# Optimization experiments

Hardware: AMD Instinct MI355X
Metric: run time of the kernel (lower is better)

Reference implementation:

```python
import jax, jax.numpy as jnp
import numpy as np

N_USER = 100000
N_RECIPE = 50000
E = 1000000
H = 128


def setup_inputs() -> dict:
    key = jax.random.key(0)
    ks = jax.random.split(key, 5)
    z_user = jax.random.normal(ks[0], (N_USER, H), dtype=jnp.float32)
    z_recipe = jax.random.normal(ks[1], (N_RECIPE, H), dtype=jnp.float32)
    edge_label_index = jax.random.randint(ks[2], (2, E), 0, N_RECIPE, dtype=jnp.int64)
    W1 = jax.random.normal(ks[3], (2 * H, H), dtype=jnp.float32) * (1.0 / np.sqrt(2 * H))
    b1 = jnp.zeros((H,), dtype=jnp.float32)
    W2 = jax.random.normal(ks[4], (H, 1), dtype=jnp.float32) * (1.0 / np.sqrt(H))
    b2 = jnp.zeros((1,), dtype=jnp.float32)
    return {"z_user": z_user, "z_recipe": z_recipe,
            "edge_label_index": edge_label_index,
            "W1": W1, "b1": b1, "W2": W2, "b2": b2}


def reference(z_user, z_recipe, edge_label_index, W1, b1, W2, b2):
    row, col = edge_label_index[0], edge_label_index[1]
    # gather + concat: [E, 2H]
    z = jnp.concatenate([z_user[row], z_recipe[col]], axis=-1)
    h = jax.nn.relu(z @ W1 + b1)        # [E, H]
    out = h @ W2 + b2                    # [E, 1]
    return out.reshape(-1)
```

## Files before the change

kernel.cpp:

```cpp
#include <hip/hip_runtime.h>
#include <hip/hip_bf16.h>


#define HDIM 128

typedef __attribute__((ext_vector_type(8))) __bf16 bf16x8;
typedef __attribute__((ext_vector_type(16))) float f32x16;

static __device__ __forceinline__ unsigned short bf16_bits(float x) {
  return __builtin_bit_cast(unsigned short, static_cast<__bf16>(x));
}

static __device__ __forceinline__ float bf2f(unsigned short u) {
  return __builtin_bit_cast(float, ((unsigned int)u) << 16);
}

static __device__ __forceinline__ bf16x8 cvt8(float4 a, float4 b) {
  bf16x8 r;
  r[0] = static_cast<__bf16>(a.x);
  r[1] = static_cast<__bf16>(a.y);
  r[2] = static_cast<__bf16>(a.z);
  r[3] = static_cast<__bf16>(a.w);
  r[4] = static_cast<__bf16>(b.x);
  r[5] = static_cast<__bf16>(b.y);
  r[6] = static_cast<__bf16>(b.z);
  r[7] = static_cast<__bf16>(b.w);
  return r;
}

__global__ __launch_bounds__(256) void prep(const float* __restrict__ W1,
                                            unsigned short* __restrict__ W1bf,
                                            const int* __restrict__ eidx, int E,
                                            int* __restrict__ maxarr) {
  const int tid = threadIdx.x;
  const int b = blockIdx.x;
  if (b < 16 && W1bf) {
#pragma unroll
    for (int it = 0; it < 8; ++it) {
      const int idx = (b << 11) + (it << 8) + tid;
      const int k = idx >> 7;
      const int n = idx & 127;
      const int kc = k >> 4;
      const int q = (k >> 3) & 1;
      const int j = k & 7;
      const int nt = n >> 5;
      const int ln = (q << 5) | (n & 31);
      W1bf[((((kc << 2) + nt) << 6) | ln) * 8 + j] = bf16_bits(W1[idx]);
    }
  }
  int local = -1;
  for (int i = b * 256 + tid; i < E; i += 64 * 256)
    local = max(local, eidx[i]);
#pragma unroll
  for (int st = 1; st <= 32; st <<= 1)
    local = max(local, __shfl_xor(local, st));
  __shared__ int wmax[4];
  if ((tid & 63) == 0) wmax[tid >> 6] = local;
  __syncthreads();
  if (tid == 0) {
    int m = max(max(wmax[0], wmax[1]), max(wmax[2], wmax[3]));
    maxarr[b] = m;
  }
}

__global__ __launch_bounds__(256, 4) void proj_nodes(
    const float* __restrict__ zu, int NU, const float* __restrict__ zr, int NR,
    const float* __restrict__ W1, const unsigned short* __restrict__ W1bf,
    const int* __restrict__ maxarr,
    unsigned short* __restrict__ Hu, unsigned short* __restrict__ Hr,
    int ublocks) {
  __shared__ unsigned short Bsw[16384];
  const int tid = threadIdx.x;
  const bool isU = (int)blockIdx.x < ublocks;
  const int kc0 = isU ? 0 : 8;

  if (W1bf) {
    const uint4* s4 = (const uint4*)(W1bf + (kc0 << 11));
    uint4* d4 = (uint4*)Bsw;
#pragma unroll
    for (int i = 0; i < 8; ++i) d4[(i << 8) + tid] = s4[(i << 8) + tid];
  } else {
    const int n = tid & 127;
    const int kh = tid >> 7;
    const int nt = n >> 5;
    const int nl = n & 31;
#pragma unroll 8
    for (int it = 0; it < 64; ++it) {
      const int kl = 2 * it + kh;
      const float w = W1[(kc0 * 16 + kl) * HDIM + n];
      const int kc = kl >> 4;
      const int q = (kl >> 3) & 1;
      const int j = kl & 7;
      const int ln = (q << 5) | nl;
      Bsw[((((kc << 2) + nt) << 6) | ln) * 8 + j] = bf16_bits(w);
    }
  }
  __syncthreads();

  const int lane = tid & 63;
  const int wid = tid >> 6;
  const int m = lane & 31;
  const int half = lane >> 5;
  const int koff = half * 8;

  const int wbase = (isU ? (int)blockIdx.x : (int)blockIdx.x - ublocks) * 4 + wid;
  const int ntiles = isU ? ((NU + 31) >> 5) : ((NR + 31) >> 5);
  const int wstride = (isU ? ublocks : ((int)gridDim.x - ublocks)) * 4;

  int vmax = 0x7fffffff;
  if (isU && maxarr) {
    int v = maxarr[lane];
#pragma unroll
    for (int st = 1; st <= 32; st <<= 1) v = max(v, __shfl_xor(v, st));
    vmax = v;
  }

  const int nmax = isU ? NU : NR;
  const float* zsrc = isU ? zu : zr;
  unsigned short* H = isU ? Hu : Hr;

  for (int t = wbase; t < ntiles; t += wstride) {
    const int base = t << 5;
    if (isU && base > vmax) continue;
    int node = base + m;
    if (node >= nmax) node = nmax - 1;
    const float* src = zsrc + (size_t)node * HDIM + koff;

    f32x16 acc[4];
#pragma unroll
    for (int nt = 0; nt < 4; ++nt) acc[nt] = (f32x16)0.0f;

#pragma unroll
    for (int kcl = 0; kcl < 8; ++kcl) {
      const float4* sa = (const float4*)(src + kcl * 16);
      const bf16x8 a = cvt8(sa[0], sa[1]);
#pragma unroll
      for (int nt = 0; nt < 4; ++nt) {
        const uint4* bp =
            (const uint4*)(Bsw + ((((kcl << 2) + nt) << 6) | lane) * 8);
        const bf16x8 bfr = __builtin_bit_cast(bf16x8, *bp);
        acc[nt] = __builtin_amdgcn_mfma_f32_32x32x16_bf16(a, bfr, acc[nt], 0, 0, 0);
      }
    }

#pragma unroll
    for (int nt = 0; nt < 4; ++nt) {
#pragma unroll
      for (int r = 0; r < 16; ++r) {
        const int row = (r & 3) + ((r >> 2) << 3) + (half << 2);
        const int nrow = base + row;
        if (nrow < nmax)
          H[(size_t)nrow * HDIM + (nt << 5) + m] = bf16_bits(acc[nt][r]);
      }
    }
  }
}

static __device__ __forceinline__ float dot8(uint4 a, uint4 b,
                                             const float* b1c,
                                             const float* w2c) {
  const unsigned short* pa = (const unsigned short*)&a;
  const unsigned short* pb = (const unsigned short*)&b;
  float s = 0.f;
#pragma unroll
  for (int j = 0; j < 8; ++j) {
    const float h = bf2f(pa[j]) + bf2f(pb[j]) + b1c[j];
    s = fmaf(fmaxf(h, 0.f), w2c[j], s);
  }
  return s;
}

__global__ __launch_bounds__(256, 4) void edge_pass(
    const unsigned short* __restrict__ Hu, const unsigned short* __restrict__ Hr,
    const int* __restrict__ eidx, const float* __restrict__ b1,
    const float* __restrict__ W2, const float* __restrict__ b2,
    float* __restrict__ out, int E, int eBeg, int eEnd) {
  const int tid = threadIdx.x;
  const int lane = tid & 63;
  const int c = lane & 15;
  const int g = lane >> 4;
  const int wid = blockIdx.x * 4 + (tid >> 6);
  const int stride = gridDim.x * 4 * 16;

  float b1c[8], w2c[8];
#pragma unroll
  for (int j = 0; j < 8; ++j) {
    b1c[j] = b1[c * 8 + j];
    w2c[j] = W2[c * 8 + j];
  }
  const float b2v = b2[0];
  const int co = c * 8;

  int e = eBeg + wid * 16 + g * 4;
  if (e >= eEnd) return;
  int iu0 = eidx[e],     ir0 = eidx[E + e];
  int iu1 = eidx[e + 1], ir1 = eidx[E + e + 1];
  int iu2 = eidx[e + 2], ir2 = eidx[E + e + 2];
  int iu3 = eidx[e + 3], ir3 = eidx[E + e + 3];

  while (true) {
    const int en = e + stride;
    const bool more = en < eEnd;
    const int ep = more ? en : e;

    const uint4 au0 = *(const uint4*)(Hu + (size_t)iu0 * HDIM + co);
    const uint4 ar0 = *(const uint4*)(Hr + (size_t)ir0 * HDIM + co);
    const uint4 au1 = *(const uint4*)(Hu + (size_t)iu1 * HDIM + co);
    const uint4 ar1 = *(const uint4*)(Hr + (size_t)ir1 * HDIM + co);
    const uint4 au2 = *(const uint4*)(Hu + (size_t)iu2 * HDIM + co);
    const uint4 ar2 = *(const uint4*)(Hr + (size_t)ir2 * HDIM + co);
    const uint4 au3 = *(const uint4*)(Hu + (size_t)iu3 * HDIM + co);
    const uint4 ar3 = *(const uint4*)(Hr + (size_t)ir3 * HDIM + co);

    const int niu0 = eidx[ep],     nir0 = eidx[E + ep];
    const int niu1 = eidx[ep + 1], nir1 = eidx[E + ep + 1];
    const int niu2 = eidx[ep + 2], nir2 = eidx[E + ep + 2];
    const int niu3 = eidx[ep + 3], nir3 = eidx[E + ep + 3];

    float s0 = dot8(au0, ar0, b1c, w2c);
    float s1 = dot8(au1, ar1, b1c, w2c);
    float s2 = dot8(au2, ar2, b1c, w2c);
    float s3 = dot8(au3, ar3, b1c, w2c);
#pragma unroll
    for (int st = 1; st <= 8; st <<= 1) {
      s0 += __shfl_xor(s0, st);
      s1 += __shfl_xor(s1, st);
      s2 += __shfl_xor(s2, st);
      s3 += __shfl_xor(s3, st);
    }
    if (c == 0) {
      out[e]     = s0 + b2v;
      out[e + 1] = s1 + b2v;
      out[e + 2] = s2 + b2v;
      out[e + 3] = s3 + b2v;
    }
    if (!more) break;
    e = en;
    iu0 = niu0; ir0 = nir0; iu1 = niu1; ir1 = nir1;
    iu2 = niu2; ir2 = nir2; iu3 = niu3; ir3 = nir3;
  }
}

__global__ __launch_bounds__(256, 2) void edge_decoder_mfma(
    const float* __restrict__ zu, const float* __restrict__ zr,
    const int* __restrict__ eidx, const float* __restrict__ W1,
    const float* __restrict__ b1, const float* __restrict__ W2,
    const float* __restrict__ b2, float* __restrict__ out, int E) {
  __shared__ unsigned short Bsw[32768];
  const int tid = threadIdx.x;
  {
    const int n = tid & 127;
    const int kh = tid >> 7;
    const int nt = n >> 5;
    const int nl = n & 31;
#pragma unroll 8
    for (int it = 0; it < 128; ++it) {
      const int k = 2 * it + kh;
      const float w = W1[k * HDIM + n];
      const int kc = k >> 4;
      const int q = (k >> 3) & 1;
      const int j = k & 7;
      const int ln = (q << 5) | nl;
      Bsw[((((kc << 2) + nt) << 6) | ln) * 8 + j] = bf16_bits(w);
    }
  }
  __syncthreads();

  const int lane = tid & 63;
  const int wid = tid >> 6;
  const int m = lane & 31;
  const int half = lane >> 5;
  const int nsweep = E >> 6;
  const int wstride = gridDim.x * 4;

  float b1v[4], w2v[4];
#pragma unroll
  for (int nt = 0; nt < 4; ++nt) {
    b1v[nt] = b1[nt * 32 + m];
    w2v[nt] = W2[nt * 32 + m];
  }
  const float b2v = b2[0];
  const int koff = half * 8;

  for (int s = blockIdx.x * 4 + wid; s < nsweep; s += wstride) {
    const int e0 = s << 6;
    const int eA = e0 + m;
    const int eB = e0 + 32 + m;
    const float* puA = zu + (size_t)eidx[eA] * HDIM;
    const float* prA = zr + (size_t)eidx[E + eA] * HDIM;
    const float* puB = zu + (size_t)eidx[eB] * HDIM;
    const float* prB = zr + (size_t)eidx[E + eB] * HDIM;

    f32x16 acc[2][4];
#pragma unroll
    for (int mt = 0; mt < 2; ++mt)
#pragma unroll
      for (int nt = 0; nt < 4; ++nt) acc[mt][nt] = (f32x16)0.0f;

#pragma unroll
    for (int kc = 0; kc < 16; ++kc) {
      const float* srcA = (kc < 8) ? (puA + kc * 16 + koff) : (prA + (kc - 8) * 16 + koff);
      const float* srcB = (kc < 8) ? (puB + kc * 16 + koff) : (prB + (kc - 8) * 16 + koff);
      const float4* sa = (const float4*)srcA;
      const float4* sb = (const float4*)srcB;
      const bf16x8 a0 = cvt8(sa[0], sa[1]);
      const bf16x8 a1 = cvt8(sb[0], sb[1]);
#pragma unroll
      for (int nt = 0; nt < 4; ++nt) {
        const uint4* bp = (const uint4*)(Bsw + ((((kc << 2) + nt) << 6) | lane) * 8);
        const bf16x8 bfr = __builtin_bit_cast(bf16x8, *bp);
        acc[0][nt] = __builtin_amdgcn_mfma_f32_32x32x16_bf16(a0, bfr, acc[0][nt], 0, 0, 0);
        acc[1][nt] = __builtin_amdgcn_mfma_f32_32x32x16_bf16(a1, bfr, acc[1][nt], 0, 0, 0);
      }
    }

    float p0[16], p1[16];
#pragma unroll
    for (int r = 0; r < 16; ++r) { p0[r] = 0.f; p1[r] = 0.f; }
#pragma unroll
    for (int nt = 0; nt < 4; ++nt) {
#pragma unroll
      for (int r = 0; r < 16; ++r) {
        float h0 = fmaxf(acc[0][nt][r] + b1v[nt], 0.f);
        float h1 = fmaxf(acc[1][nt][r] + b1v[nt], 0.f);
        p0[r] = fmaf(h0, w2v[nt], p0[r]);
        p1[r] = fmaf(h1, w2v[nt], p1[r]);
      }
    }
#pragma unroll
    for (int st = 1; st <= 16; st <<= 1) {
#pragma unroll
      for (int r = 0; r < 16; ++r) {
        p0[r] += __shfl_xor(p0[r], st);
        p1[r] += __shfl_xor(p1[r], st);
      }
    }
    const int sel = lane & 15;
    const int mtw = (lane >> 4) & 1;
    float val = 0.f;
#pragma unroll
    for (int r = 0; r < 16; ++r) {
      const float cand = mtw ? p1[r] : p0[r];
      val = (sel == r) ? cand : val;
    }
    const int mrow = (sel & 3) + ((sel >> 2) << 3) + (half << 2);
    out[e0 + (mtw << 5) + mrow] = val + b2v;
  }
}

extern "C" void kernel_launch(void* const* d_in, const int* in_sizes, int n_in,
                              void* d_out, int out_size, void* d_ws,
                              size_t ws_size, hipStream_t stream) {
  const float* zu = (const float*)d_in[0];
  const float* zr = (const float*)d_in[1];
  const int* eidx = (const int*)d_in[2];
  const float* W1 = (const float*)d_in[3];
  const float* b1 = (const float*)d_in[4];
  const float* W2 = (const float*)d_in[5];
  const float* b2 = (const float*)d_in[6];
  float* out = (float*)d_out;
  const int nu = in_sizes[0];
  const int nr = in_sizes[1];
  const int E = in_sizes[2] / 2;
  const int NU = nu / HDIM, NR = nr / HDIM;

  const size_t needH = (size_t)(nu + nr) * sizeof(unsigned short);
  const size_t needW = 32768 * sizeof(unsigned short);
  const size_t needM = 64 * sizeof(int);

  if (ws_size >= needH) {
    unsigned short* Hu = (unsigned short*)d_ws;
    unsigned short* Hr = Hu + (size_t)nu;
    unsigned short* W1bf = nullptr;
    int* maxarr = nullptr;
    if (ws_size >= needH + needW + needM) {
      W1bf = Hr + (size_t)nr;
      maxarr = (int*)(W1bf + 32768);
      hipLaunchKernelGGL(prep, dim3(64), dim3(256), 0, stream,
                         W1, W1bf, eidx, E, maxarr);
    }
    const int utiles = (NU + 31) >> 5;
    const int rtiles = (NR + 31) >> 5;
    const int ub = (utiles + 7) >> 3;
    const int rb = (rtiles + 7) >> 3;
    hipLaunchKernelGGL(proj_nodes, dim3(ub + rb), dim3(256), 0, stream,
                       zu, NU, zr, NR, W1, W1bf, maxarr, Hu, Hr, ub);
    const int half = (E >> 1) & ~15;
    hipLaunchKernelGGL(edge_pass, dim3(2048), dim3(256), 0, stream,
                       Hu, Hr, eidx, b1, W2, b2, out, E, 0, half);
    hipLaunchKernelGGL(edge_pass, dim3(2048), dim3(256), 0, stream,
                       Hu, Hr, eidx, b1, W2, b2, out, E, half, E);
  } else {
    hipLaunchKernelGGL(edge_decoder_mfma, dim3(512), dim3(256), 0, stream,
                       zu, zr, eidx, W1, b1, W2, b2, out, E);
  }
}
```

Before: 196.1 us.

## Bin edges by row/col stripe so each XCD gathers a cache-resident slice

Adds a histogram and scatter pass that sorts edges into 8x8 bins by row and column index stripes. The edge kernel then assigns each row-stripe group to one XCD via blockIdx&7, so each XCD's L2 serves a smaller slice of the projected node tables. The goal is to cut random HBM gather traffic. In exchange it adds two extra kernels, about 12 MB of index writes and reads, scattered output writes through sid, and a heavier prep pass that also computes column maxima. The proj_nodes grid sizing also changes (ub/rb divisor from 8 to 4).

```diff
diff --git a/kernel.cpp b/kernel.cpp
--- a/kernel.cpp
+++ b/kernel.cpp
@@ -28,6 +28,23 @@
   return r;
 }
 
+static __device__ __forceinline__ int stripe8(int x, int xmax) {
+  return (int)(((long long)x << 3) / ((long long)xmax + 1));
+}
+
+static __device__ __forceinline__ void load_maxes(const int* maxarr, int lane,
+                                                  int& rmax, int& cmax) {
+  int rv = maxarr[lane];
+  int cv = maxarr[64 + lane];
+#pragma unroll
+  for (int st = 1; st <= 32; st <<= 1) {
+    rv = max(rv, __shfl_xor(rv, st));
+    cv = max(cv, __shfl_xor(cv, st));
+  }
+  rmax = rv;
+  cmax = cv;
+}
+
 __global__ __launch_bounds__(256) void prep(const float* __restrict__ W1,
                                             unsigned short* __restrict__ W1bf,
                                             const int* __restrict__ eidx, int E,
@@ -48,18 +65,92 @@
       W1bf[((((kc << 2) + nt) << 6) | ln) * 8 + j] = bf16_bits(W1[idx]);
     }
   }
-  int local = -1;
-  for (int i = b * 256 + tid; i < E; i += 64 * 256)
-    local = max(local, eidx[i]);
-#pragma unroll
-  for (int st = 1; st <= 32; st <<= 1)
-    local = max(local, __shfl_xor(local, st));
-  __shared__ int wmax[4];
-  if ((tid & 63) == 0) wmax[tid >> 6] = local;
+  int lr = -1, lc = -1;
+  for (int i = b * 256 + tid; i < E; i += 64 * 256) {
+    lr = max(lr, eidx[i]);
+    lc = max(lc, eidx[E + i]);
+  }
+#pragma unroll
+  for (int st = 1; st <= 32; st <<= 1) {
+    lr = max(lr, __shfl_xor(lr, st));
+    lc = max(lc, __shfl_xor(lc, st));
+  }
+  __shared__ int wr[4], wc[4];
+  if ((tid & 63) == 0) {
+    wr[tid >> 6] = lr;
+    wc[tid >> 6] = lc;
+  }
   __syncthreads();
   if (tid == 0) {
-    int m = max(max(wmax[0], wmax[1]), max(wmax[2], wmax[3]));
-    maxarr[b] = m;
+    maxarr[b] = max(max(wr[0], wr[1]), max(wr[2], wr[3]));
+    maxarr[64 + b] = max(max(wc[0], wc[1]), max(wc[2], wc[3]));
+  }
+}
+
+__global__ __launch_bounds__(256) void khist(const int* __restrict__ eidx,
+                                             int E,
+                                             const int* __restrict__ maxarr,
+                                             int* __restrict__ blockhist) {
+  const int tid = threadIdx.x;
+  const int b = blockIdx.x;
+  int rmax, cmax;
+  load_maxes(maxarr, tid & 63, rmax, cmax);
+  __shared__ int h[64];
+  if (tid < 64) h[tid] = 0;
+  __syncthreads();
+  for (int i = b * 256 + tid; i < E; i += 64 * 256) {
+    const int bin = stripe8(eidx[i], rmax) * 8 + stripe8(eidx[E + i], cmax);
+    atomicAdd(&h[bin], 1);
+  }
+  __syncthreads();
+  if (tid < 64) blockhist[b * 64 + tid] = h[tid];
+}
+
+__global__ __launch_bounds__(256) void kscatter(
+    const int* __restrict__ eidx, int E, const int* __restrict__ maxarr,
+    const int* __restrict__ blockhist, int* __restrict__ srow,
+    int* __restrict__ scol, int* __restrict__ sid, int* __restrict__ binstart) {
+  const int tid = threadIdx.x;
+  const int b = blockIdx.x;
+  int rmax, cmax;
+  load_maxes(maxarr, tid & 63, rmax, cmax);
+  __shared__ int bh[4096];
+  __shared__ int tot[64], scanT[64], offs[64];
+  for (int k = tid; k < 4096; k += 256) bh[k] = blockhist[k];
+  __syncthreads();
+  int mine = 0;
+  if (tid < 64) {
+    int t = 0;
+    for (int bb = 0; bb < 64; ++bb) {
+      const int v = bh[bb * 64 + tid];
+      if (bb < b) mine += v;
+      t += v;
+    }
+    tot[tid] = t;
+  }
+  __syncthreads();
+  if (tid == 0) {
+    int run = 0;
+    for (int k = 0; k < 64; ++k) {
+      scanT[k] = run;
+      run += tot[k];
+    }
+  }
+  __syncthreads();
+  if (tid < 64) offs[tid] = scanT[tid] + mine;
+  if (b == 0) {
+    if (tid < 64) binstart[tid] = scanT[tid];
+    if (tid == 0) binstart[64] = E;
+  }
+  __syncthreads();
+  for (int i = b * 256 + tid; i < E; i += 64 * 256) {
+    const int r = eidx[i];
+    const int cc = eidx[E + i];
+    const int bin = stripe8(r, rmax) * 8 + stripe8(cc, cmax);
+    const int pos = atomicAdd(&offs[bin], 1);
+    srow[pos] = r;
+    scol[pos] = cc;
+    sid[pos] = i;
   }
 }
 
@@ -170,11 +261,82 @@
   return s;
 }
 
+__global__ __launch_bounds__(256, 4) void edge_binned(
+    const unsigned short* __restrict__ Hu, const unsigned short* __restrict__ Hr,
+    const int* __restrict__ srow, const int* __restrict__ scol,
+    const int* __restrict__ sid, const int* __restrict__ binstart,
+    const float* __restrict__ b1, const float* __restrict__ W2,
+    const float* __restrict__ b2, float* __restrict__ out) {
+  const int tid = threadIdx.x;
+  const int lane = tid & 63;
+  const int c = lane & 15;
+  const int g = lane >> 4;
+  const int xcd = (int)blockIdx.x & 7;
+  const int segbeg = binstart[xcd << 3];
+  const int segend = binstart[(xcd << 3) + 8];
+  if (segbeg >= segend) return;
+
+  float b1c[8], w2c[8];
+#pragma unroll
+  for (int j = 0; j < 8; ++j) {
+    b1c[j] = b1[c * 8 + j];
+    w2c[j] = W2[c * 8 + j];
+  }
+  const float b2v = b2[0];
+  const int co = c * 8;
+
+  const int nw = ((int)gridDim.x >> 3) * 4;
+  const int widx = (((int)blockIdx.x >> 3) << 2) + (tid >> 6);
+  const int wstride = nw * 16;
+
+  for (int base = segbeg + widx * 16; base < segend; base += wstride) {
+    const int r0 = base + (g << 2);
+    int i0 = r0, i1 = r0 + 1, i2 = r0 + 2, i3 = r0 + 3;
+    const bool v0 = i0 < segend, v1 = i1 < segend;
+    const bool v2 = i2 < segend, v3 = i3 < segend;
+    if (!v0) i0 = segbeg;
+    if (!v1) i1 = segbeg;
+    if (!v2) i2 = segbeg;
+    if (!v3) i3 = segbeg;
+    const int iu0 = srow[i0], ir0 = scol[i0];
+    const int iu1 = srow[i1], ir1 = scol[i1];
+    const int iu2 = srow[i2], ir2 = scol[i2];
+    const int iu3 = srow[i3], ir3 = scol[i3];
+
+    const uint4 au0 = *(const uint4*)(Hu + (size_t)iu0 * HDIM + co);
+    const uint4 ar0 = *(const uint4*)(Hr + (size_t)ir0 * HDIM + co);
+    const uint4 au1 = *(const uint4*)(Hu + (size_t)iu1 * HDIM + co);
+    const uint4 ar1 = *(const uint4*)(Hr + (size_t)ir1 * HDIM + co);
+    const uint4 au2 = *(const uint4*)(Hu + (size_t)iu2 * HDIM + co);
+    const uint4 ar2 = *(const uint4*)(Hr + (size_t)ir2 * HDIM + co);
+    const uint4 au3 = *(const uint4*)(Hu + (size_t)iu3 * HDIM + co);
+    const uint4 ar3 = *(const uint4*)(Hr + (size_t)ir3 * HDIM + co);
+
+    float s0 = dot8(au0, ar0, b1c, w2c);
+    float s1 = dot8(au1, ar1, b1c, w2c);
+    float s2 = dot8(au2, ar2, b1c, w2c);
+    float s3 = dot8(au3, ar3, b1c, w2c);
+#pragma unroll
+    for (int st = 1; st <= 8; st <<= 1) {
+      s0 += __shfl_xor(s0, st);
+      s1 += __shfl_xor(s1, st);
+      s2 += __shfl_xor(s2, st);
+      s3 += __shfl_xor(s3, st);
+    }
+    if (c == 0) {
+      if (v0) out[sid[i0]] = s0 + b2v;
+      if (v1) out[sid[i1]] = s1 + b2v;
+      if (v2) out[sid[i2]] = s2 + b2v;
+      if (v3) out[sid[i3]] = s3 + b2v;
+    }
+  }
+}
+
 __global__ __launch_bounds__(256, 4) void edge_pass(
     const unsigned short* __restrict__ Hu, const unsigned short* __restrict__ Hr,
     const int* __restrict__ eidx, const float* __restrict__ b1,
     const float* __restrict__ W2, const float* __restrict__ b2,
-    float* __restrict__ out, int E, int eBeg, int eEnd) {
+    float* __restrict__ out, int E) {
   const int tid = threadIdx.x;
   const int lane = tid & 63;
   const int c = lane & 15;
@@ -191,8 +353,8 @@
   const float b2v = b2[0];
   const int co = c * 8;
 
-  int e = eBeg + wid * 16 + g * 4;
-  if (e >= eEnd) return;
+  int e = wid * 16 + g * 4;
+  if (e >= E) return;
   int iu0 = eidx[e],     ir0 = eidx[E + e];
   int iu1 = eidx[e + 1], ir1 = eidx[E + e + 1];
   int iu2 = eidx[e + 2], ir2 = eidx[E + e + 2];
@@ -200,7 +362,7 @@
 
   while (true) {
     const int en = e + stride;
-    const bool more = en < eEnd;
+    const bool more = en < E;
     const int ep = more ? en : e;
 
     const uint4 au0 = *(const uint4*)(Hu + (size_t)iu0 * HDIM + co);
@@ -364,32 +526,49 @@
   const int E = in_sizes[2] / 2;
   const int NU = nu / HDIM, NR = nr / HDIM;
 
-  const size_t needH = (size_t)(nu + nr) * sizeof(unsigned short);
-  const size_t needW = 32768 * sizeof(unsigned short);
-  const size_t needM = 64 * sizeof(int);
-
-  if (ws_size >= needH) {
-    unsigned short* Hu = (unsigned short*)d_ws;
-    unsigned short* Hr = Hu + (size_t)nu;
-    unsigned short* W1bf = nullptr;
-    int* maxarr = nullptr;
-    if (ws_size >= needH + needW + needM) {
-      W1bf = Hr + (size_t)nr;
-      maxarr = (int*)(W1bf + 32768);
-      hipLaunchKernelGGL(prep, dim3(64), dim3(256), 0, stream,
-                         W1, W1bf, eidx, E, maxarr);
-    }
-    const int utiles = (NU + 31) >> 5;
-    const int rtiles = (NR + 31) >> 5;
-    const int ub = (utiles + 7) >> 3;
-    const int rb = (rtiles + 7) >> 3;
+  char* w = (char*)d_ws;
+  unsigned short* Hu = (unsigned short*)w;   w += (size_t)nu * 2;
+  unsigned short* Hr = (unsigned short*)w;   w += (size_t)nr * 2;
+  unsigned short* W1bf = (unsigned short*)w; w += 65536;
+  int* maxarr = (int*)w;                     w += 512;
+  int* blockhist = (int*)w;                  w += 16384;
+  int* binstart = (int*)w;                   w += 512;
+  int* srow = (int*)w;                       w += (size_t)E * 4;
+  int* scol = (int*)w;                       w += (size_t)E * 4;
+  int* sid = (int*)w;                        w += (size_t)E * 4;
+  const size_t needFull = (size_t)(w - (char*)d_ws);
+  const size_t needH = (size_t)(nu + nr) * 2;
+  const size_t needMid = needH + 65536 + 512;
+
+  const int utiles = (NU + 31) >> 5;
+  const int rtiles = (NR + 31) >> 5;
+  const int ub = (utiles + 3) >> 2;
+  const int rb = (rtiles + 3) >> 2;
+
+  if (ws_size >= needFull) {
+    hipLaunchKernelGGL(prep, dim3(64), dim3(256), 0, stream,
+                       W1, W1bf, eidx, E, maxarr);
+    hipLaunchKernelGGL(khist, dim3(64), dim3(256), 0, stream,
+                       eidx, E, maxarr, blockhist);
+    hipLaunchKernelGGL(kscatter, dim3(64), dim3(256), 0, stream,
+                       eidx, E, maxarr, blockhist, srow, scol, sid, binstart);
     hipLaunchKernelGGL(proj_nodes, dim3(ub + rb), dim3(256), 0, stream,
                        zu, NU, zr, NR, W1, W1bf, maxarr, Hu, Hr, ub);
-    const int half = (E >> 1) & ~15;
+    hipLaunchKernelGGL(edge_binned, dim3(2048), dim3(256), 0, stream,
+                       Hu, Hr, srow, scol, sid, binstart, b1, W2, b2, out);
+  } else if (ws_size >= needH) {
+    unsigned short* W1bf2 = nullptr;
+    int* maxarr2 = nullptr;
+    if (ws_size >= needMid) {
+      W1bf2 = W1bf;
+      maxarr2 = maxarr;
+      hipLaunchKernelGGL(prep, dim3(64), dim3(256), 0, stream,
+                         W1, W1bf2, eidx, E, maxarr2);
+    }
+    hipLaunchKernelGGL(proj_nodes, dim3(ub + rb), dim3(256), 0, stream,
+                       zu, NU, zr, NR, W1, W1bf2, maxarr2, Hu, Hr, ub);
     hipLaunchKernelGGL(edge_pass, dim3(2048), dim3(256), 0, stream,
-                       Hu, Hr, eidx, b1, W2, b2, out, E, 0, half);
-    hipLaunchKernelGGL(edge_pass, dim3(2048), dim3(256), 0, stream,
-                       Hu, Hr, eidx, b1, W2, b2, out, E, half, E);
+                       Hu, Hr, eidx, b1, W2, b2, out, E);
   } else {
     hipLaunchKernelGGL(edge_decoder_mfma, dim3(512), dim3(256), 0, stream,
                        zu, zr, eidx, W1, b1, W2, b2, out, E);
```

Result: slower. 253.0 us (+29.1%).
